# Kernel optimization log

Measured on AMD Instinct MI355X. Metric: run time of the kernel, lower is better.

Reference implementation:

```python
import jax, jax.numpy as jnp
import numpy as np
from jax import lax

O, C, K = 256, 64, 3          # out_channels, in_channels, kernel size
M = 9                          # ALSH augmentation terms (m)
EXTRA = M // (K * K)           # channels Q appends to the input (=1)
D = C + EXTRA                  # d = in_channels + m/(k*k)
T = 8192                       # table_size
R = 4.0                        # hash bucket width hash.r
STRIDE, PAD = 1, 1


def _P(kernels):
    # ALSH preprocessing: flatten each kernel and append powers of its squared norm
    flat = kernels.reshape(O, -1)                        # [O, C*K*K]
    n2 = jnp.sum(flat * flat, axis=1, keepdims=True)     # [O, 1]
    pows = jnp.concatenate([n2 ** (i + 1) for i in range(M)], axis=1)  # [O, M]
    return jnp.concatenate([flat, pows], axis=1)         # [O, C*K*K + M]


def _hash(a, b, x):
    # x: [n, C*K*K + M];  floor((a . x + b) / r)
    return jnp.floor((x @ a + b) / R)


def setup_inputs():
    key = jax.random.key(0)
    k1, k2, k3, k4 = jax.random.split(key, 4)
    inp = jax.random.normal(k1, (16, C, 256, 256), jnp.float32)
    kernels = jax.random.normal(k2, (O, C, K, K), jnp.float32) * 0.04
    a = jax.random.normal(k3, (D * K * K,), jnp.float32)
    b = jax.random.uniform(k4, (1,), jnp.float32) * R
    return {"input": inp, "kernels": kernels, "a": a, "b": b}


def reference(input, kernels, a, b):
    N, _, H, W = input.shape
    # ---- init_table: hash every kernel into a bucket (vectorized scatter) ----
    hk = _hash(a, b[0], _P(kernels))                     # [O]
    idx = jnp.abs(jnp.fmod(hk, T)).astype(jnp.int32)     # torch: fmod_ then abs_
    onehot = jax.nn.one_hot(idx, T, dtype=jnp.int32)     # [O, T]
    excl = jnp.cumsum(onehot, axis=0) - onehot           # slot within bucket (insertion order)
    pos = jnp.take_along_axis(excl, idx[:, None], axis=1)[:, 0]
    table = jnp.zeros((T, 2 * O), jnp.int32).at[idx, pos].set(
        jnp.arange(O, dtype=jnp.int32))
    row_len = jnp.sum(onehot, axis=0)                    # [T] bucket sizes
    # ---- vote: hash every conv patch via a 1-output-channel convolution ----
    inp_q = jnp.concatenate(
        [input, jnp.full((N, EXTRA, H, W), 0.5, input.dtype)], axis=1)  # Q(input)
    kern = a.reshape(1, D, K, K)
    dotted = lax.conv_general_dilated(inp_q, kern, (STRIDE, STRIDE),
                                      [(PAD, PAD), (PAD, PAD)])
    votes = jnp.floor((dotted.reshape(-1) + b[0]) / R)   # [N*H'*W']
    vidx = jnp.abs(jnp.fmod(votes, T)).astype(jnp.int32)
    count = jax.ops.segment_sum(jnp.ones_like(votes), vidx, num_segments=T)
    index = jnp.argmax(count)
    # ---- gather active set (fixed-size padded gather, sorted rows) ----
    L = row_len[index]
    slot = jnp.arange(2 * O)
    rows = jnp.where(slot < L, table[index], O)          # sentinel O sorts to the end
    rows = jnp.sort(rows)
    valid = (slot < L).astype(kernels.dtype)
    active = kernels[jnp.clip(rows, 0, O - 1)] * valid[:, None, None, None]
    return active, count, index.astype(jnp.int32)
```

## Files before the change

### kernel.cpp

```cpp
#include <hip/hip_runtime.h>

#define O_CH   256
#define C_CH   64
#define FLATK  576
#define M_TERMS 9
#define AL     585
#define TSZ    8192
#define RADIUS 4.0f
#define NB     16
#define HH     256
#define WW     256

#define WS_KIDX 0
#define WS_HIST 256
#define WS_BEST (256 + TSZ)
#define WS_ROWS (256 + TSZ + 1)

__global__ __launch_bounds__(256) void k_init(const float* __restrict__ kernels,
                                              const float* __restrict__ a,
                                              const float* __restrict__ b,
                                              int* __restrict__ ws) {
    if (blockIdx.x < 64) {
        const int wv = threadIdx.x >> 6, lane = threadIdx.x & 63;
        const int o = blockIdx.x * 4 + wv;
        const float* wp = kernels + o * FLATK;
        float dot = 0.f, n2 = 0.f;
        #pragma unroll
        for (int j0 = 0; j0 < FLATK; j0 += 64) {
            float x = wp[j0 + lane];
            dot += x * a[j0 + lane];
            n2  += x * x;
        }
        #pragma unroll
        for (int off = 32; off > 0; off >>= 1) {
            dot += __shfl_xor(dot, off);
            n2  += __shfl_xor(n2, off);
        }
        if (lane == 0) {
            float p = n2, d = dot;
            for (int i = 0; i < M_TERMS; ++i) { d += p * a[FLATK + i]; p *= n2; }
            float hk = floorf((d + b[0]) / RADIUS);
            ws[WS_KIDX + o] = (int)fabsf(fmodf(hk, (float)TSZ));
        }
    } else {
        int t = (blockIdx.x - 64) * 256 + threadIdx.x;
        ws[WS_HIST + t] = 0;
    }
}

#define TILE_H 16
__global__ __launch_bounds__(512) void k_vote(const float* __restrict__ input,
                                              const float* __restrict__ a,
                                              const float* __restrict__ b,
                                              int* __restrict__ ws) {
    __shared__ int   hist_s[TSZ];
    __shared__ float a_s[AL];
    const int tid = threadIdx.x;

    for (int i = tid; i < TSZ; i += 512) hist_s[i] = 0;
    for (int i = tid; i < AL; i += 512) a_s[i] = a[i];
    __syncthreads();

    const float bv = b[0];
    const int t   = (blockIdx.x & 7) * 32 + (blockIdx.x >> 3);
    const int by  = t & 15;
    const int n   = t >> 4;
    const int y0  = by * TILE_H;
    const int lane = tid & 63;
    const int yg  = tid >> 6;
    const int x4  = lane * 4;
    const int ybase = y0 + yg * 2;

    float acc[2][4] = {{0.f,0.f,0.f,0.f},{0.f,0.f,0.f,0.f}};
    const float* imgbase = input + (size_t)n * C_CH * HH * WW;

    float4 vbuf[2][4];
    #pragma unroll
    for (int r = 0; r < 4; ++r) {
        int gy = ybase - 1 + r;
        vbuf[0][r] = (gy >= 0 && gy < HH)
                   ? *(const float4*)(imgbase + gy * WW + x4)
                   : make_float4(0.f, 0.f, 0.f, 0.f);
    }

    #pragma unroll 2
    for (int c = 0; c < C_CH; ++c) {
        const int cur = c & 1, nxt = cur ^ 1;
        if (c + 1 < C_CH) {
            const float* src = imgbase + (size_t)(c + 1) * (HH * WW);
            #pragma unroll
            for (int r = 0; r < 4; ++r) {
                int gy = ybase - 1 + r;
                vbuf[nxt][r] = (gy >= 0 && gy < HH)
                             ? *(const float4*)(src + gy * WW + x4)
                             : make_float4(0.f, 0.f, 0.f, 0.f);
            }
        }
        float win[4][6];
        #pragma unroll
        for (int r = 0; r < 4; ++r) {
            float4 v = vbuf[cur][r];
            float lv = __shfl_up(v.w, 1);   if (lane == 0)  lv = 0.f;
            float rv = __shfl_down(v.x, 1); if (lane == 63) rv = 0.f;
            win[r][0] = lv; win[r][1] = v.x; win[r][2] = v.y;
            win[r][3] = v.z; win[r][4] = v.w; win[r][5] = rv;
        }
        const float* ac = a_s + c * 9;
        #pragma unroll
        for (int rr = 0; rr < 2; ++rr)
            #pragma unroll
            for (int ky = 0; ky < 3; ++ky)
                #pragma unroll
                for (int p = 0; p < 4; ++p)
                    #pragma unroll
                    for (int kx = 0; kx < 3; ++kx)
                        acc[rr][p] += win[rr + ky][p + kx] * ac[ky * 3 + kx];
    }

    #pragma unroll
    for (int rr = 0; rr < 2; ++rr) {
        int gy = ybase + rr;
        #pragma unroll
        for (int p = 0; p < 4; ++p) {
            int gx = x4 + p;
            float cs = 0.f;
            #pragma unroll
            for (int ky = 0; ky < 3; ++ky) {
                int yy = gy + ky - 1;
                if (yy < 0 || yy >= HH) continue;
                #pragma unroll
                for (int kx = 0; kx < 3; ++kx) {
                    int xx = gx + kx - 1;
                    if (xx < 0 || xx >= WW) continue;
                    cs += a_s[FLATK + ky * 3 + kx];
                }
            }
            float tt = acc[rr][p] + 0.5f * cs;
            float v = floorf((tt + bv) / RADIUS);
            int vi = (int)fabsf(fmodf(v, (float)TSZ));
            atomicAdd(&hist_s[vi], 1);
        }
    }

    __syncthreads();
    int* hist_g = ws + WS_HIST;
    for (int i = tid; i < TSZ; i += 512) {
        int v = hist_s[i];
        if (v) atomicAdd(&hist_g[i], v);
    }
}

__global__ __launch_bounds__(256) void k_finalize(int* __restrict__ ws,
                                                  float* __restrict__ out) {
    __shared__ int sv[256], si[256];
    __shared__ int wsum[4];
    const int tid = threadIdx.x;
    const int* hist = ws + WS_HIST;

    int best = -1, bidx = 0;
    for (int t = tid; t < TSZ; t += 256) {
        int v = hist[t];
        if (v > best) { best = v; bidx = t; }
    }
    sv[tid] = best; si[tid] = bidx;
    __syncthreads();
    for (int s = 128; s > 0; s >>= 1) {
        if (tid < s) {
            if (sv[tid + s] > sv[tid] ||
                (sv[tid + s] == sv[tid] && si[tid + s] < si[tid])) {
                sv[tid] = sv[tid + s]; si[tid] = si[tid + s];
            }
        }
        __syncthreads();
    }
    const int bestIdx = si[0];

    float* count_out = out + 512 * FLATK;
    for (int t = tid; t < TSZ; t += 256) count_out[t] = (float)hist[t];
    if (tid == 0) {
        out[512 * FLATK + TSZ] = (float)bestIdx;
        ws[WS_BEST] = bestIdx;
    }

    int* rows = ws + WS_ROWS;
    for (int i = tid; i < 2 * O_CH; i += 256) rows[i] = -1;
    const int o = tid;
    const int match = (ws[WS_KIDX + o] == bestIdx) ? 1 : 0;
    unsigned long long m = __ballot(match);
    const int lane = tid & 63, wv = tid >> 6;
    if (lane == 0) wsum[wv] = __popcll(m);
    __syncthreads();
    int prefix = 0;
    for (int i = 0; i < wv; ++i) prefix += wsum[i];
    int before = __popcll(m & ((1ull << lane) - 1ull));
    if (match) rows[prefix + before] = o;
}

__global__ void k_gather(const float* __restrict__ kernels,
                         const int* __restrict__ ws,
                         float* __restrict__ out) {
    int gid = blockIdx.x * blockDim.x + threadIdx.x;
    if (gid >= 2 * O_CH * FLATK) return;
    int s = gid / FLATK;
    int j = gid - s * FLATK;
    int r = ws[WS_ROWS + s];
    out[gid] = (r >= 0) ? kernels[r * FLATK + j] : 0.0f;
}

extern "C" void kernel_launch(void* const* d_in, const int* in_sizes, int n_in,
                              void* d_out, int out_size, void* d_ws, size_t ws_size,
                              hipStream_t stream) {
    const float* input   = (const float*)d_in[0];
    const float* kernels = (const float*)d_in[1];
    const float* a       = (const float*)d_in[2];
    const float* b       = (const float*)d_in[3];
    float* out = (float*)d_out;
    int*   ws  = (int*)d_ws;

    k_init<<<96, 256, 0, stream>>>(kernels, a, b, ws);
    k_vote<<<NB * (HH / TILE_H), 512, 0, stream>>>(input, a, b, ws);
    k_finalize<<<1, 256, 0, stream>>>(ws, out);
    k_gather<<<(2 * O_CH * FLATK + 255) / 256, 256, 0, stream>>>(kernels, ws, out);
}
```

Measured before the change: 405.6 us.

## Smaller vote tiles, deeper prefetch, parallel argmax, vectorized gather

The vote kernel now gives each wavefront one output row (TILE_H 8, 512 blocks) with a four-slot, two-channel-ahead prefetch ring and an occupancy hint in launch bounds. The single-block argmax is replaced by a multi-block reduction that packs count and reversed index into a 64-bit key and combines blocks with atomicMax, followed by a separate kernel that builds the row list. The gather kernel moves to float4 loads and stores. The smaller tiles double the halo loads (three input rows per output row instead of four per two), and the extra kernel launch adds a little fixed cost.

New measurement: 426.2 us. +5.1%, slower.

```diff
diff --git a/kernel.cpp b/kernel.cpp
--- a/kernel.cpp
+++ b/kernel.cpp
@@ -14,7 +14,7 @@
 #define WS_KIDX 0
 #define WS_HIST 256
 #define WS_BEST (256 + TSZ)
-#define WS_ROWS (256 + TSZ + 1)
+#define WS_ROWS (256 + TSZ + 2)
 
 __global__ __launch_bounds__(256) void k_init(const float* __restrict__ kernels,
                                               const float* __restrict__ a,
@@ -45,14 +45,15 @@
     } else {
         int t = (blockIdx.x - 64) * 256 + threadIdx.x;
         ws[WS_HIST + t] = 0;
-    }
-}
-
-#define TILE_H 16
-__global__ __launch_bounds__(512) void k_vote(const float* __restrict__ input,
-                                              const float* __restrict__ a,
-                                              const float* __restrict__ b,
-                                              int* __restrict__ ws) {
+        if (blockIdx.x == 64 && threadIdx.x < 2) ws[WS_BEST + threadIdx.x] = 0;
+    }
+}
+
+#define TILE_H 8
+__global__ __launch_bounds__(512, 4) void k_vote(const float* __restrict__ input,
+                                                 const float* __restrict__ a,
+                                                 const float* __restrict__ b,
+                                                 int* __restrict__ ws) {
     __shared__ int   hist_s[TSZ];
     __shared__ float a_s[AL];
     const int tid = threadIdx.x;
@@ -62,43 +63,48 @@
     __syncthreads();
 
     const float bv = b[0];
-    const int t   = (blockIdx.x & 7) * 32 + (blockIdx.x >> 3);
-    const int by  = t & 15;
-    const int n   = t >> 4;
+    const int t   = (blockIdx.x & 7) * 64 + (blockIdx.x >> 3);
+    const int by  = t & 31;
+    const int n   = t >> 5;
     const int y0  = by * TILE_H;
     const int lane = tid & 63;
-    const int yg  = tid >> 6;
+    const int wv  = tid >> 6;
     const int x4  = lane * 4;
-    const int ybase = y0 + yg * 2;
-
-    float acc[2][4] = {{0.f,0.f,0.f,0.f},{0.f,0.f,0.f,0.f}};
+    const int y   = y0 + wv;
+
+    float acc[4] = {0.f, 0.f, 0.f, 0.f};
     const float* imgbase = input + (size_t)n * C_CH * HH * WW;
 
-    float4 vbuf[2][4];
+    float4 vbuf[4][3];
     #pragma unroll
-    for (int r = 0; r < 4; ++r) {
-        int gy = ybase - 1 + r;
-        vbuf[0][r] = (gy >= 0 && gy < HH)
-                   ? *(const float4*)(imgbase + gy * WW + x4)
-                   : make_float4(0.f, 0.f, 0.f, 0.f);
-    }
-
-    #pragma unroll 2
+    for (int cc = 0; cc < 2; ++cc) {
+        const float* src = imgbase + (size_t)cc * (HH * WW);
+        #pragma unroll
+        for (int r = 0; r < 3; ++r) {
+            int gy = y - 1 + r;
+            vbuf[cc][r] = (gy >= 0 && gy < HH)
+                        ? *(const float4*)(src + gy * WW + x4)
+                        : make_float4(0.f, 0.f, 0.f, 0.f);
+        }
+    }
+
+    #pragma unroll 4
     for (int c = 0; c < C_CH; ++c) {
-        const int cur = c & 1, nxt = cur ^ 1;
-        if (c + 1 < C_CH) {
-            const float* src = imgbase + (size_t)(c + 1) * (HH * WW);
+        const int cur = c & 3;
+        if (c + 2 < C_CH) {
+            const float* src = imgbase + (size_t)(c + 2) * (HH * WW);
+            const int nx = (c + 2) & 3;
             #pragma unroll
-            for (int r = 0; r < 4; ++r) {
-                int gy = ybase - 1 + r;
-                vbuf[nxt][r] = (gy >= 0 && gy < HH)
-                             ? *(const float4*)(src + gy * WW + x4)
-                             : make_float4(0.f, 0.f, 0.f, 0.f);
+            for (int r = 0; r < 3; ++r) {
+                int gy = y - 1 + r;
+                vbuf[nx][r] = (gy >= 0 && gy < HH)
+                            ? *(const float4*)(src + gy * WW + x4)
+                            : make_float4(0.f, 0.f, 0.f, 0.f);
             }
         }
-        float win[4][6];
-        #pragma unroll
-        for (int r = 0; r < 4; ++r) {
+        float win[3][6];
+        #pragma unroll
+        for (int r = 0; r < 3; ++r) {
             float4 v = vbuf[cur][r];
             float lv = __shfl_up(v.w, 1);   if (lane == 0)  lv = 0.f;
             float rv = __shfl_down(v.x, 1); if (lane == 63) rv = 0.f;
@@ -107,19 +113,16 @@
         }
         const float* ac = a_s + c * 9;
         #pragma unroll
-        for (int rr = 0; rr < 2; ++rr)
+        for (int ky = 0; ky < 3; ++ky)
             #pragma unroll
-            for (int ky = 0; ky < 3; ++ky)
+            for (int p = 0; p < 4; ++p)
                 #pragma unroll
-                for (int p = 0; p < 4; ++p)
-                    #pragma unroll
-                    for (int kx = 0; kx < 3; ++kx)
-                        acc[rr][p] += win[rr + ky][p + kx] * ac[ky * 3 + kx];
-    }
-
-    #pragma unroll
-    for (int rr = 0; rr < 2; ++rr) {
-        int gy = ybase + rr;
+                for (int kx = 0; kx < 3; ++kx)
+                    acc[p] += win[ky][p + kx] * ac[ky * 3 + kx];
+    }
+
+    {
+        int gy = y;
         #pragma unroll
         for (int p = 0; p < 4; ++p) {
             int gx = x4 + p;
@@ -135,7 +138,7 @@
                     cs += a_s[FLATK + ky * 3 + kx];
                 }
             }
-            float tt = acc[rr][p] + 0.5f * cs;
+            float tt = acc[p] + 0.5f * cs;
             float v = floorf((tt + bv) / RADIUS);
             int vi = (int)fabsf(fmodf(v, (float)TSZ));
             atomicAdd(&hist_s[vi], 1);
@@ -150,61 +153,65 @@
     }
 }
 
-__global__ __launch_bounds__(256) void k_finalize(int* __restrict__ ws,
-                                                  float* __restrict__ out) {
-    __shared__ int sv[256], si[256];
+__global__ __launch_bounds__(256) void k_argmax(const int* __restrict__ ws,
+                                                int* __restrict__ wsbest,
+                                                float* __restrict__ out) {
+    const int tid = threadIdx.x;
+    const int t = blockIdx.x * 256 + tid;
+    const int v = ws[WS_HIST + t];
+    out[512 * FLATK + t] = (float)v;
+
+    unsigned long long key =
+        ((unsigned long long)(unsigned)v << 13) | (unsigned)(TSZ - 1 - t);
+    #pragma unroll
+    for (int off = 32; off > 0; off >>= 1) {
+        unsigned long long o = __shfl_xor(key, off);
+        if (o > key) key = o;
+    }
+    __shared__ unsigned long long wk[4];
+    const int lane = tid & 63, wvi = tid >> 6;
+    if (lane == 0) wk[wvi] = key;
+    __syncthreads();
+    if (tid == 0) {
+        unsigned long long k = wk[0];
+        for (int i = 1; i < 4; ++i) if (wk[i] > k) k = wk[i];
+        atomicMax((unsigned long long*)(wsbest + WS_BEST), k);
+    }
+}
+
+__global__ __launch_bounds__(256) void k_rows(int* __restrict__ ws,
+                                              float* __restrict__ out) {
     __shared__ int wsum[4];
     const int tid = threadIdx.x;
-    const int* hist = ws + WS_HIST;
-
-    int best = -1, bidx = 0;
-    for (int t = tid; t < TSZ; t += 256) {
-        int v = hist[t];
-        if (v > best) { best = v; bidx = t; }
-    }
-    sv[tid] = best; si[tid] = bidx;
-    __syncthreads();
-    for (int s = 128; s > 0; s >>= 1) {
-        if (tid < s) {
-            if (sv[tid + s] > sv[tid] ||
-                (sv[tid + s] == sv[tid] && si[tid + s] < si[tid])) {
-                sv[tid] = sv[tid + s]; si[tid] = si[tid + s];
-            }
-        }
-        __syncthreads();
-    }
-    const int bestIdx = si[0];
-
-    float* count_out = out + 512 * FLATK;
-    for (int t = tid; t < TSZ; t += 256) count_out[t] = (float)hist[t];
-    if (tid == 0) {
-        out[512 * FLATK + TSZ] = (float)bestIdx;
-        ws[WS_BEST] = bestIdx;
-    }
+    const unsigned long long key = *(const unsigned long long*)(ws + WS_BEST);
+    const int bestIdx = (TSZ - 1) - (int)(key & (unsigned long long)(TSZ - 1));
+    if (tid == 0) out[512 * FLATK + TSZ] = (float)bestIdx;
 
     int* rows = ws + WS_ROWS;
     for (int i = tid; i < 2 * O_CH; i += 256) rows[i] = -1;
     const int o = tid;
     const int match = (ws[WS_KIDX + o] == bestIdx) ? 1 : 0;
     unsigned long long m = __ballot(match);
-    const int lane = tid & 63, wv = tid >> 6;
-    if (lane == 0) wsum[wv] = __popcll(m);
+    const int lane = tid & 63, wvi = tid >> 6;
+    if (lane == 0) wsum[wvi] = __popcll(m);
     __syncthreads();
     int prefix = 0;
-    for (int i = 0; i < wv; ++i) prefix += wsum[i];
+    for (int i = 0; i < wvi; ++i) prefix += wsum[i];
     int before = __popcll(m & ((1ull << lane) - 1ull));
     if (match) rows[prefix + before] = o;
 }
 
-__global__ void k_gather(const float* __restrict__ kernels,
-                         const int* __restrict__ ws,
-                         float* __restrict__ out) {
-    int gid = blockIdx.x * blockDim.x + threadIdx.x;
-    if (gid >= 2 * O_CH * FLATK) return;
-    int s = gid / FLATK;
-    int j = gid - s * FLATK;
+__global__ __launch_bounds__(256) void k_gather(const float* __restrict__ kernels,
+                                                const int* __restrict__ ws,
+                                                float* __restrict__ out) {
+    int gid = blockIdx.x * 256 + threadIdx.x;
+    if (gid >= 2 * O_CH * (FLATK / 4)) return;
+    int s = gid / (FLATK / 4);
+    int j = gid - s * (FLATK / 4);
     int r = ws[WS_ROWS + s];
-    out[gid] = (r >= 0) ? kernels[r * FLATK + j] : 0.0f;
+    float4 v = (r >= 0) ? *(const float4*)(kernels + r * FLATK + j * 4)
+                        : make_float4(0.f, 0.f, 0.f, 0.f);
+    *((float4*)out + gid) = v;
 }
 
 extern "C" void kernel_launch(void* const* d_in, const int* in_sizes, int n_in,
@@ -219,6 +226,7 @@
 
     k_init<<<96, 256, 0, stream>>>(kernels, a, b, ws);
     k_vote<<<NB * (HH / TILE_H), 512, 0, stream>>>(input, a, b, ws);
-    k_finalize<<<1, 256, 0, stream>>>(ws, out);
-    k_gather<<<(2 * O_CH * FLATK + 255) / 256, 256, 0, stream>>>(kernels, ws, out);
-}
+    k_argmax<<<TSZ / 256, 256, 0, stream>>>(ws, ws, out);
+    k_rows<<<1, 256, 0, stream>>>(ws, out);
+    k_gather<<<(2 * O_CH * (FLATK / 4) + 255) / 256, 256, 0, stream>>>(kernels, ws, out);
+}
```
